# Optimization experiments

Measured on AMD Instinct MI355X. Metric: run time of the kernel, lower is better.

The kernel has to match this reference:

```python
import jax, jax.numpy as jnp
import numpy as np

B, N, K, D = 16, 16384, 16, 256  # batch, num feature tokens, num slots, slot/feature dim
FEAT = 256
LN_EPS = 1e-5


def _ln(x, g, b):
    m = jnp.mean(x, -1, keepdims=True)
    v = jnp.mean((x - m) ** 2, -1, keepdims=True)
    return (x - m) * jax.lax.rsqrt(v + LN_EPS) * g + b


def setup_inputs() -> dict:
    key = jax.random.key(0)
    ks = jax.random.split(key, 18)
    s = 0.02
    return {
        "features": jax.random.normal(ks[0], (B, N, FEAT), jnp.float32),
        "slots_init": jax.random.normal(ks[1], (B, K, D), jnp.float32),
        "g_f": jnp.ones((FEAT,), jnp.float32), "b_f": jnp.zeros((FEAT,), jnp.float32),
        "g_s": jnp.ones((D,), jnp.float32), "b_s": jnp.zeros((D,), jnp.float32),
        "g_m": jnp.ones((D,), jnp.float32), "b_m": jnp.zeros((D,), jnp.float32),
        "Wq": jax.random.normal(ks[2], (D, D), jnp.float32) * s,
        "Wk": jax.random.normal(ks[3], (D, FEAT), jnp.float32) * s,
        "Wv": jax.random.normal(ks[4], (D, FEAT), jnp.float32) * s,
        "w_ih": jax.random.normal(ks[5], (3 * D, D), jnp.float32) * s,
        "w_hh": jax.random.normal(ks[6], (3 * D, D), jnp.float32) * s,
        "b_ih": jnp.zeros((3 * D,), jnp.float32),
        "b_hh": jnp.zeros((3 * D,), jnp.float32),
        "W1": jax.random.normal(ks[7], (4 * D, D), jnp.float32) * s,
        "b1": jnp.zeros((4 * D,), jnp.float32),
        "W2": jax.random.normal(ks[8], (D, 4 * D), jnp.float32) * s,
        "b2": jnp.zeros((D,), jnp.float32),
        "num_src_view": 4,
    }


def reference(features, slots_init, g_f, b_f, g_s, b_s, g_m, b_m, Wq, Wk, Wv,
              w_ih, w_hh, b_ih, b_hh, W1, b1, W2, b2, num_src_view):
    f = _ln(features, g_f, b_f)            # [B,N,FEAT]
    k = f @ Wk.T                            # [B,N,D]
    v = f @ Wv.T                            # [B,N,D]
    scale = float(D) ** -0.5                # num_head = 1, head-mean is identity

    def gru(x, h):  # PyTorch GRUCell math, batched over [B,K]
        gi = x @ w_ih.T + b_ih
        gh = h @ w_hh.T + b_hh
        ir, iz, inn = jnp.split(gi, 3, -1)
        hr, hz, hn = jnp.split(gh, 3, -1)
        r = jax.nn.sigmoid(ir + hr)
        z = jax.nn.sigmoid(iz + hz)
        n = jnp.tanh(inn + r * hn)
        return (1.0 - z) * n + z * h

    def one_iter(slots):
        q = _ln(slots, g_s, b_s) @ Wq.T                         # [B,K,D]
        logits = jnp.einsum('bkd,bnd->bkn', q, k) * scale       # [B,K,N]
        attn = jax.nn.softmax(logits, axis=1)                   # competitive over slots
        attn_wm = attn / (jnp.sum(attn, -1, keepdims=True) + 1.0)  # epsilon = 1.0
        updates = jnp.einsum('bkn,bnd->bkd', attn_wm, v)        # [B,K,D]
        h = gru(updates, slots)
        h = h + (jax.nn.relu(_ln(h, g_m, b_m) @ W1.T + b1) @ W2.T + b2)
        return h, attn

    slots = slots_init
    for _ in range(2):  # num_iter - 1 iterations with straight-through detach trick
        slots, _ = one_iter(slots)
        slots = jax.lax.stop_gradient(slots) + slots_init - jax.lax.stop_gradient(slots_init)
    slots, attn = one_iter(slots)
    return slots, attn
```

## Files before the change

### kernel.cpp

```cpp
#include <hip/hip_runtime.h>
#include <cstdint>
#include <cstddef>

#define BB    16
#define NTOK  16384
#define KS    16
#define DD    256
#define FEATN 256
#define NBLK  32
#define LN_EPS 1e-5f

typedef float        float4v __attribute__((ext_vector_type(4)));
typedef unsigned int uint4v  __attribute__((ext_vector_type(4)));
typedef unsigned int uint2v  __attribute__((ext_vector_type(2)));
typedef __bf16       bf16x8  __attribute__((ext_vector_type(8)));

__device__ __forceinline__ float bflo(unsigned u){ return __builtin_bit_cast(float, u << 16); }
__device__ __forceinline__ float bfhi(unsigned u){ return __builtin_bit_cast(float, u & 0xffff0000u); }
__device__ __forceinline__ unsigned short f2bf(float v){ __bf16 b = (__bf16)v; return __builtin_bit_cast(unsigned short, b); }
__device__ __forceinline__ float sigm(float x){ return 1.f/(1.f + __expf(-x)); }

__global__ void prep_w_kernel(const float* __restrict__ Wv, const float* __restrict__ w_ih,
                              const float* __restrict__ w_hh, const float* __restrict__ W1,
                              const float* __restrict__ W2, const float* __restrict__ Wq,
                              const float* __restrict__ Wk,
                              unsigned short* __restrict__ Wv_t, unsigned short* __restrict__ wih_t,
                              unsigned short* __restrict__ whh_t, unsigned short* __restrict__ W1_t,
                              unsigned short* __restrict__ W2_t, unsigned short* __restrict__ Wq_t,
                              unsigned short* __restrict__ Wk_b)
{
  __shared__ float tile[64][65];
  const int t = blockIdx.x, tid = threadIdx.x;
  const float* src; unsigned short* dst; int R, C, base;
  if      (t < 16)  { src = Wv;   dst = Wv_t;  R = 256;  C = 256;  base = 0;   }
  else if (t < 64)  { src = w_ih; dst = wih_t; R = 768;  C = 256;  base = 16;  }
  else if (t < 112) { src = w_hh; dst = whh_t; R = 768;  C = 256;  base = 64;  }
  else if (t < 176) { src = W1;   dst = W1_t;  R = 1024; C = 256;  base = 112; }
  else if (t < 240) { src = W2;   dst = W2_t;  R = 256;  C = 1024; base = 176; }
  else if (t < 256) { src = Wq;   dst = Wq_t;  R = 256;  C = 256;  base = 240; }
  else {
    const int t2 = t - 256;
    for (int i = tid; i < 4096; i += 256) {
      const int idx = t2*4096 + i;
      Wk_b[idx] = f2bf(Wk[idx]);
    }
    return;
  }
  const int tt = t - base;
  const int tiles_r = R >> 6;
  const int r0 = (tt % tiles_r) * 64, c0 = (tt / tiles_r) * 64;
  const int j = tid & 63, i0 = (tid >> 6) * 16;
  for (int s = 0; s < 16; ++s)
    tile[i0 + s][j] = src[(size_t)(r0 + i0 + s)*C + c0 + j];
  __syncthreads();
  for (int s = 0; s < 16; ++s) {
    const int i = i0 + s;
    dst[(size_t)(c0 + i)*R + r0 + j] = f2bf(tile[j][i]);
  }
}

__device__ __forceinline__ void lnqu_tail_p(
    const float* Vs, float* Ys, float* Qs, float* Pp, float* SUb, float* CBb,
    const float* __restrict__ g_s, const float* __restrict__ b_s,
    const unsigned short* __restrict__ Wq_t, const unsigned short* __restrict__ Wk_b,
    const float* __restrict__ g_f, const float* __restrict__ b_f,
    unsigned short* __restrict__ u_buf, float* __restrict__ su_buf, float* __restrict__ cb_buf,
    int b, int k0, int tid)
{
  const int w = tid >> 6, L = tid & 63;
  {
    const float v0 = Vs[w*256+L], v1 = Vs[w*256+64+L], v2 = Vs[w*256+128+L], v3 = Vs[w*256+192+L];
    float s = v0+v1+v2+v3;
    #pragma unroll
    for (int m = 1; m < 64; m <<= 1) s += __shfl_xor(s, m);
    const float mean = s * (1.f/DD);
    const float d0 = v0-mean, d1 = v1-mean, d2 = v2-mean, d3 = v3-mean;
    float s2 = d0*d0 + d1*d1 + d2*d2 + d3*d3;
    #pragma unroll
    for (int m = 1; m < 64; m <<= 1) s2 += __shfl_xor(s2, m);
    const float rs = rsqrtf(s2 * (1.f/DD) + LN_EPS);
    Ys[L*4+w]       = d0*rs*g_s[L]      + b_s[L];
    Ys[(64+L)*4+w]  = d1*rs*g_s[64+L]   + b_s[64+L];
    Ys[(128+L)*4+w] = d2*rs*g_s[128+L]  + b_s[128+L];
    Ys[(192+L)*4+w] = d3*rs*g_s[192+L]  + b_s[192+L];
  }
  __syncthreads();
  {
    float acc[4][4] = {};
    for (int cc = w*64; cc < w*64+64; ++cc) {
      const float4v xv = *reinterpret_cast<const float4v*>(Ys + cc*4);
      const uint2v wr = *reinterpret_cast<const uint2v*>(Wq_t + (size_t)cc*DD + 4*L);
      const float w0 = bflo(wr[0]), w1 = bfhi(wr[0]), w2 = bflo(wr[1]), w3 = bfhi(wr[1]);
      #pragma unroll
      for (int s = 0; s < 4; ++s) {
        acc[s][0] += xv[s]*w0; acc[s][1] += xv[s]*w1;
        acc[s][2] += xv[s]*w2; acc[s][3] += xv[s]*w3;
      }
    }
    #pragma unroll
    for (int s = 0; s < 4; ++s)
      *reinterpret_cast<float4v*>(Pp + (w*4+s)*256 + 4*L) = *reinterpret_cast<const float4v*>(acc[s]);
  }
  __syncthreads();
  for (int i = tid; i < 4*DD; i += 256) {
    const int kk = i >> 8, d = i & 255;
    Qs[d*4+kk] = Pp[(0*4+kk)*256+d] + Pp[(1*4+kk)*256+d] + Pp[(2*4+kk)*256+d] + Pp[(3*4+kk)*256+d];
  }
  __syncthreads();
  {
    float acc[4][4] = {};
    for (int d = w*64; d < w*64+64; ++d) {
      const float4v xv = *reinterpret_cast<const float4v*>(Qs + d*4);
      const uint2v wr = *reinterpret_cast<const uint2v*>(Wk_b + (size_t)d*DD + 4*L);
      const float w0 = bflo(wr[0]), w1 = bfhi(wr[0]), w2 = bflo(wr[1]), w3 = bfhi(wr[1]);
      #pragma unroll
      for (int s = 0; s < 4; ++s) {
        acc[s][0] += xv[s]*w0; acc[s][1] += xv[s]*w1;
        acc[s][2] += xv[s]*w2; acc[s][3] += xv[s]*w3;
      }
    }
    #pragma unroll
    for (int s = 0; s < 4; ++s)
      *reinterpret_cast<float4v*>(Pp + (w*4+s)*256 + 4*L) = *reinterpret_cast<const float4v*>(acc[s]);
  }
  __syncthreads();
  for (int i = tid; i < 4*DD; i += 256) {
    const int kk = i >> 8, cc = i & 255;
    const float qk = Pp[(0*4+kk)*256+cc] + Pp[(1*4+kk)*256+cc] + Pp[(2*4+kk)*256+cc] + Pp[(3*4+kk)*256+cc];
    const float uv = qk * g_f[cc];
    u_buf[(size_t)(b*KS + k0 + kk)*DD + cc] = f2bf(uv);
    SUb[kk*256+cc] = uv;
    CBb[kk*256+cc] = qk * b_f[cc];
  }
  __syncthreads();
  {
    float s  = SUb[w*256+L] + SUb[w*256+64+L] + SUb[w*256+128+L] + SUb[w*256+192+L];
    float cv = CBb[w*256+L] + CBb[w*256+64+L] + CBb[w*256+128+L] + CBb[w*256+192+L];
    #pragma unroll
    for (int m = 1; m < 64; m <<= 1) { s += __shfl_xor(s, m); cv += __shfl_xor(cv, m); }
    if (L == 0) { su_buf[b*KS + k0 + w] = s; cb_buf[b*KS + k0 + w] = cv; }
  }
}

__global__ void k0_kernel(const float* __restrict__ slots_init,
                          const float* __restrict__ g_s, const float* __restrict__ b_s,
                          const unsigned short* __restrict__ Wq_t, const unsigned short* __restrict__ Wk_b,
                          const float* __restrict__ g_f, const float* __restrict__ b_f,
                          unsigned short* __restrict__ u_buf, float* __restrict__ su_buf,
                          float* __restrict__ cb_buf)
{
  const int b = blockIdx.x >> 2, k0 = (blockIdx.x & 3) * 4;
  const int tid = threadIdx.x;
  __shared__ __align__(16) float Vs[4*DD];
  __shared__ __align__(16) float Ys[DD*4];
  __shared__ __align__(16) float Qs[DD*4];
  __shared__ __align__(16) float Pp[4*4*DD];
  __shared__ __align__(16) float SUb[4*DD];
  __shared__ __align__(16) float CBb[4*DD];
  for (int i = tid; i < 4*DD; i += 256)
    Vs[i] = slots_init[(size_t)(b*KS + k0)*DD + i];
  __syncthreads();
  lnqu_tail_p(Vs, Ys, Qs, Pp, SUb, CBb, g_s, b_s, Wq_t, Wk_b, g_f, b_f,
              u_buf, su_buf, cb_buf, b, k0, tid);
}

template<int MODE, int LAST>
__launch_bounds__(256, 2)
__global__ void phaseA_kernel(const float* __restrict__ feat,
                              unsigned short* __restrict__ xb, float* __restrict__ stats,
                              const unsigned short* __restrict__ u_buf,
                              const float* __restrict__ su_buf,
                              const float* __restrict__ cb_buf,
                              float* __restrict__ P_part,
                              float* __restrict__ S_part,
                              float* __restrict__ R_part,
                              float* __restrict__ attn_out)
{
  __shared__ __align__(16) unsigned int xl[4][128*36];
  __shared__ float ssh[4][16];
  __shared__ float rsh[4][16];

  const int b   = blockIdx.x / NBLK;
  const int blk = blockIdx.x - b*NBLK;
  const int tid = threadIdx.x;
  const int w = tid >> 6;
  const int l = tid & 63;
  const int c = l & 15;
  const int g = l >> 4;

  bf16x8 ufrag[8];
  {
    const bf16x8* up = reinterpret_cast<const bf16x8*>(u_buf + (size_t)(b*KS + c)*DD);
    #pragma unroll
    for (int kk = 0; kk < 8; ++kk) ufrag[kk] = up[4*kk + g];
  }
  const float su_c = su_buf[b*KS + c];
  const float cb_c = cb_buf[b*KS + c];

  float4v Pacc[16];
  #pragma unroll
  for (int t = 0; t < 16; ++t) Pacc[t] = (float4v){0.f,0.f,0.f,0.f};
  float S_acc = 0.f, R_acc = 0.f;

  unsigned int* myxl = xl[w];
  const int rbase = 8*(c>>2) + (c&3);

  for (int pass = 0; pass < 4; ++pass) {
    const int n0 = blk*(NTOK/NBLK) + pass*128 + w*32;
    float4v Ct[2];
    float m_t[2], rs_t[2];

    if constexpr (MODE == 1) {
      bf16x8 xr0[8], xr1[8];
      float2 st0, st1;
      {
        const size_t row0 = (size_t)b*NTOK + (size_t)(n0 + rbase);
        const size_t row1 = row0 + 4;
        const bf16x8* p0v = reinterpret_cast<const bf16x8*>(xb + row0*FEATN);
        const bf16x8* p1v = reinterpret_cast<const bf16x8*>(xb + row1*FEATN);
        #pragma unroll
        for (int kk = 0; kk < 8; ++kk) { xr0[kk] = p0v[4*kk + g]; xr1[kk] = p1v[4*kk + g]; }
        st0 = *reinterpret_cast<const float2*>(stats + row0*2);
        st1 = *reinterpret_cast<const float2*>(stats + row1*2);
      }
      #pragma unroll
      for (int tp = 0; tp < 2; ++tp) {
        const int nloc = rbase + 4*tp;
        float4v Cacc = (float4v){0.f,0.f,0.f,0.f};
        #pragma unroll
        for (int kk = 0; kk < 8; ++kk) {
          const bf16x8 af = tp ? xr1[kk] : xr0[kk];
          const uint4v ad = __builtin_bit_cast(uint4v, af);
          const int pb = (16*kk + 4*g)*36 + nloc;
          myxl[pb      ] = ad[0];
          myxl[pb + 36 ] = ad[1];
          myxl[pb + 72 ] = ad[2];
          myxl[pb + 108] = ad[3];
          Cacc = __builtin_amdgcn_mfma_f32_16x16x32_bf16(af, ufrag[kk], Cacc, 0, 0, 0);
        }
        m_t[tp]  = tp ? st1.x : st0.x;
        rs_t[tp] = tp ? st1.y : st0.y;
        Ct[tp]   = Cacc;
      }
    } else {
      #pragma unroll
      for (int tp = 0; tp < 2; ++tp) {
        const int nloc = rbase + 4*tp;
        const size_t row = (size_t)b*NTOK + (size_t)(n0 + nloc);
        const float* fr = feat + row*FEATN;
        float4v xf[16];
        #pragma unroll
        for (int kk = 0; kk < 8; ++kk) {
          xf[2*kk]   = *reinterpret_cast<const float4v*>(fr + 32*kk + 8*g);
          xf[2*kk+1] = *reinterpret_cast<const float4v*>(fr + 32*kk + 8*g + 4);
        }
        unsigned short* xw = xb + row*FEATN;
        float sum = 0.f, sq = 0.f;
        float4v Cacc = (float4v){0.f,0.f,0.f,0.f};
        #pragma unroll
        for (int kk = 0; kk < 8; ++kk) {
          const float4v x0 = xf[2*kk], x1 = xf[2*kk+1];
          sum += x0[0]+x0[1]+x0[2]+x0[3] + x1[0]+x1[1]+x1[2]+x1[3];
          sq  += x0[0]*x0[0]+x0[1]*x0[1]+x0[2]*x0[2]+x0[3]*x0[3]
               + x1[0]*x1[0]+x1[1]*x1[1]+x1[2]*x1[2]+x1[3]*x1[3];
          bf16x8 af;
          af[0]=(__bf16)x0[0]; af[1]=(__bf16)x0[1]; af[2]=(__bf16)x0[2]; af[3]=(__bf16)x0[3];
          af[4]=(__bf16)x1[0]; af[5]=(__bf16)x1[1]; af[6]=(__bf16)x1[2]; af[7]=(__bf16)x1[3];
          *reinterpret_cast<bf16x8*>(xw + 32*kk + 8*g) = af;
          const uint4v ad = __builtin_bit_cast(uint4v, af);
          const int pb = (16*kk + 4*g)*36 + nloc;
          myxl[pb      ] = ad[0];
          myxl[pb + 36 ] = ad[1];
          myxl[pb + 72 ] = ad[2];
          myxl[pb + 108] = ad[3];
          Cacc = __builtin_amdgcn_mfma_f32_16x16x32_bf16(af, ufrag[kk], Cacc, 0, 0, 0);
        }
        sum += __shfl_xor(sum,16); sum += __shfl_xor(sum,32);
        sq  += __shfl_xor(sq ,16); sq  += __shfl_xor(sq ,32);
        const float mean = sum * (1.f/FEATN);
        const float var  = sq  * (1.f/FEATN) - mean*mean;
        m_t[tp]  = mean;
        rs_t[tp] = rsqrtf(var + LN_EPS);
        float2 st; st.x = m_t[tp]; st.y = rs_t[tp];
        *reinterpret_cast<float2*>(stats + row*2) = st;
        Ct[tp] = Cacc;
      }
    }

    float arr[8];
    #pragma unroll
    for (int tp = 0; tp < 2; ++tp) {
      float lv[4], rsr[4], mr[4];
      #pragma unroll
      for (int r = 0; r < 4; ++r) {
        const int src = 4*g + r;
        rsr[r] = __shfl(rs_t[tp], src);
        mr[r]  = __shfl(m_t[tp],  src);
        lv[r]  = 0.0625f * (rsr[r]*(Ct[tp][r] - mr[r]*su_c) + cb_c);
      }
      float a_[4];
      #pragma unroll
      for (int r = 0; r < 4; ++r) {
        float v = lv[r];
        v = fmaxf(v, __shfl_xor(v,1));
        v = fmaxf(v, __shfl_xor(v,2));
        v = fmaxf(v, __shfl_xor(v,4));
        v = fmaxf(v, __shfl_xor(v,8));
        const float e = __expf(lv[r] - v);
        float s = e;
        s += __shfl_xor(s,1);
        s += __shfl_xor(s,2);
        s += __shfl_xor(s,4);
        s += __shfl_xor(s,8);
        const float a = e / s;
        a_[r] = a;
        S_acc += a;
        R_acc += a * rsr[r] * mr[r];
        arr[4*tp + r] = a * rsr[r];
      }
      if (LAST) {
        float4v av = {a_[0], a_[1], a_[2], a_[3]};
        *reinterpret_cast<float4v*>(attn_out + (size_t)(b*KS + c)*NTOK + (size_t)(n0 + 8*g + 4*tp)) = av;
      }
    }
    bf16x8 afrag;
    #pragma unroll
    for (int j = 0; j < 8; ++j) afrag[j] = (__bf16)arr[j];

    #pragma unroll
    for (int t = 0; t < 16; ++t) {
      const unsigned int* rp = &myxl[(t*8 + (c>>1))*36 + 8*g];
      const uint4v q0 = *reinterpret_cast<const uint4v*>(rp);
      const uint4v q1 = *reinterpret_cast<const uint4v*>(rp + 4);
      const unsigned int sel = (c & 1) ? 0x07060302u : 0x05040100u;
      uint4v bd;
      bd[0] = __builtin_amdgcn_perm(q0[1], q0[0], sel);
      bd[1] = __builtin_amdgcn_perm(q0[3], q0[2], sel);
      bd[2] = __builtin_amdgcn_perm(q1[1], q1[0], sel);
      bd[3] = __builtin_amdgcn_perm(q1[3], q1[2], sel);
      const bf16x8 bfrag = __builtin_bit_cast(bf16x8, bd);
      Pacc[t] = __builtin_amdgcn_mfma_f32_16x16x32_bf16(afrag, bfrag, Pacc[t], 0, 0, 0);
    }
  }

  S_acc += __shfl_xor(S_acc,16); S_acc += __shfl_xor(S_acc,32);
  R_acc += __shfl_xor(R_acc,16); R_acc += __shfl_xor(R_acc,32);
  if (g == 0) { ssh[w][c] = S_acc; rsh[w][c] = R_acc; }

  float* pf = reinterpret_cast<float*>(myxl);
  #pragma unroll
  for (int t = 0; t < 16; ++t) {
    #pragma unroll
    for (int r = 0; r < 4; ++r) pf[(4*g + r)*256 + t*16 + c] = Pacc[t][r];
  }
  __syncthreads();
  {
    float* outp = P_part + (size_t)blockIdx.x * (KS*DD);
    const float* p0 = reinterpret_cast<const float*>(&xl[0][0]);
    const float* p1 = p0 + 4608;
    const float* p2 = p0 + 9216;
    const float* p3 = p0 + 13824;
    for (int i = tid; i < KS*DD; i += 256) outp[i] = p0[i]+p1[i]+p2[i]+p3[i];
    if (tid < KS) {
      S_part[blockIdx.x*KS + tid] = ssh[0][tid]+ssh[1][tid]+ssh[2][tid]+ssh[3][tid];
      R_part[blockIdx.x*KS + tid] = rsh[0][tid]+rsh[1][tid]+rsh[2][tid]+rsh[3][tid];
    }
  }
}

template<int LAST, int NEXT>
__global__ void fusedB_kernel(const float* __restrict__ P_part, const float* __restrict__ S_part,
                              const float* __restrict__ R_part, const float* __restrict__ slots_in,
                              const float* __restrict__ g_f, const float* __restrict__ b_f,
                              const unsigned short* __restrict__ Wv_t,
                              const unsigned short* __restrict__ wih_t,
                              const unsigned short* __restrict__ whh_t,
                              const float* __restrict__ b_ih, const float* __restrict__ b_hh,
                              const float* __restrict__ g_m, const float* __restrict__ b_m,
                              const unsigned short* __restrict__ W1_t, const float* __restrict__ b1,
                              const unsigned short* __restrict__ W2_t, const float* __restrict__ b2v,
                              const float* __restrict__ g_s, const float* __restrict__ b_s,
                              const unsigned short* __restrict__ Wq_t,
                              const unsigned short* __restrict__ Wk_b,
                              float* __restrict__ slots_next, float* __restrict__ out_slots,
                              unsigned short* __restrict__ u_buf, float* __restrict__ su_buf,
                              float* __restrict__ cb_buf)
{
  const int b = blockIdx.x >> 4, k = blockIdx.x & 15;
  const int tid = threadIdx.x;
  const int w = tid >> 6, L = tid & 63;

  __shared__ __align__(16) float arena[9984];
  __shared__ float SRsh[2];
  __shared__ float redsh[8];

  float* Pp    = arena;
  float* Hsh   = arena + 6144;
  float* Tsh   = arena + 6400;
  float* Ush   = arena + 6656;
  float* Gish  = arena + 6912;
  float* Ghsh  = arena + 7680;
  float* Hpsh  = arena + 8448;
  float* Ysh   = arena + 8704;
  float* Hidsh = arena + 8960;

  Hsh[tid] = slots_in[(size_t)(b*KS + k)*DD + tid];
  if (tid < 64) {
    const int p = tid & 31;
    const float* sp = (tid < 32) ? S_part : R_part;
    float v = sp[(b*NBLK + p)*KS + k];
    v += __shfl_xor(v, 1); v += __shfl_xor(v, 2); v += __shfl_xor(v, 4);
    v += __shfl_xor(v, 8); v += __shfl_xor(v, 16);
    if (p == 0) SRsh[tid >> 5] = v;
  }
  __syncthreads();

  {
    const float S = SRsh[0], R = SRsh[1];
    const float inv = 1.f / (S + 1.f);
    const float* pb = P_part + (size_t)(b*NBLK)*KS*DD + (size_t)k*DD + tid;
    float p0 = 0.f, p1 = 0.f, p2 = 0.f, p3 = 0.f;
    #pragma unroll
    for (int p = 0; p < NBLK; p += 4) {
      p0 += pb[(size_t)(p+0)*KS*DD];
      p1 += pb[(size_t)(p+1)*KS*DD];
      p2 += pb[(size_t)(p+2)*KS*DD];
      p3 += pb[(size_t)(p+3)*KS*DD];
    }
    const float P = (p0 + p1) + (p2 + p3);
    Tsh[tid] = (g_f[tid]*(P - R) + S*b_f[tid]) * inv;
  }
  __syncthreads();

  {
    const int c0 = 4*L;
    float a0 = 0.f, a1 = 0.f, a2 = 0.f, a3 = 0.f;
    for (int cc = w*64; cc < w*64+64; ++cc) {
      const float x = Tsh[cc];
      const uint2v wr = *reinterpret_cast<const uint2v*>(Wv_t + (size_t)cc*DD + c0);
      a0 += x*bflo(wr[0]); a1 += x*bfhi(wr[0]);
      a2 += x*bflo(wr[1]); a3 += x*bfhi(wr[1]);
    }
    float4v av = {a0, a1, a2, a3};
    *reinterpret_cast<float4v*>(Pp + w*256 + c0) = av;
  }
  __syncthreads();
  Ush[tid] = Pp[tid] + Pp[256+tid] + Pp[512+tid] + Pp[768+tid];
  __syncthreads();

  {
    const int c0 = 4*L;
    float ai[3][4] = {}, ah[3][4] = {};
    for (int cc = w*64; cc < w*64+64; ++cc) {
      const float xi = Ush[cc], xh = Hsh[cc];
      #pragma unroll
      for (int c = 0; c < 3; ++c) {
        const uint2v wi = *reinterpret_cast<const uint2v*>(wih_t + (size_t)cc*768 + c0 + 256*c);
        const uint2v wh = *reinterpret_cast<const uint2v*>(whh_t + (size_t)cc*768 + c0 + 256*c);
        ai[c][0] += xi*bflo(wi[0]); ai[c][1] += xi*bfhi(wi[0]);
        ai[c][2] += xi*bflo(wi[1]); ai[c][3] += xi*bfhi(wi[1]);
        ah[c][0] += xh*bflo(wh[0]); ah[c][1] += xh*bfhi(wh[0]);
        ah[c][2] += xh*bflo(wh[1]); ah[c][3] += xh*bfhi(wh[1]);
      }
    }
    #pragma unroll
    for (int c = 0; c < 3; ++c) {
      *reinterpret_cast<float4v*>(Pp + w*768 + 256*c + c0)        = *reinterpret_cast<const float4v*>(ai[c]);
      *reinterpret_cast<float4v*>(Pp + 3072 + w*768 + 256*c + c0) = *reinterpret_cast<const float4v*>(ah[c]);
    }
  }
  __syncthreads();
  for (int j = tid; j < 768; j += 256) {
    Gish[j] = b_ih[j] + Pp[j] + Pp[768+j] + Pp[1536+j] + Pp[2304+j];
    Ghsh[j] = b_hh[j] + Pp[3072+j] + Pp[3840+j] + Pp[4608+j] + Pp[5376+j];
  }
  __syncthreads();

  {
    const int d = tid;
    const float r = sigm(Gish[d] + Ghsh[d]);
    const float z = sigm(Gish[256+d] + Ghsh[256+d]);
    const float n = tanhf(Gish[512+d] + r*Ghsh[512+d]);
    const float hp = (1.f - z)*n + z*Hsh[d];
    Hpsh[d] = hp;
    float s = hp;
    #pragma unroll
    for (int m = 1; m < 64; m <<= 1) s += __shfl_xor(s, m);
    if (L == 0) redsh[w] = s;
    __syncthreads();
    const float mean = (redsh[0]+redsh[1]+redsh[2]+redsh[3]) * (1.f/DD);
    const float dv = hp - mean;
    float s2 = dv*dv;
    #pragma unroll
    for (int m = 1; m < 64; m <<= 1) s2 += __shfl_xor(s2, m);
    if (L == 0) redsh[4+w] = s2;
    __syncthreads();
    const float var = (redsh[4]+redsh[5]+redsh[6]+redsh[7]) * (1.f/DD);
    Ysh[d] = dv * rsqrtf(var + LN_EPS) * g_m[d] + b_m[d];
  }
  __syncthreads();

  {
    const int c0 = 4*L;
    float a[4][4] = {};
    for (int cc = w*64; cc < w*64+64; ++cc) {
      const float x = Ysh[cc];
      #pragma unroll
      for (int c = 0; c < 4; ++c) {
        const uint2v wr = *reinterpret_cast<const uint2v*>(W1_t + (size_t)cc*1024 + c0 + 256*c);
        a[c][0] += x*bflo(wr[0]); a[c][1] += x*bfhi(wr[0]);
        a[c][2] += x*bflo(wr[1]); a[c][3] += x*bfhi(wr[1]);
      }
    }
    #pragma unroll
    for (int c = 0; c < 4; ++c)
      *reinterpret_cast<float4v*>(Pp + w*1024 + 256*c + c0) = *reinterpret_cast<const float4v*>(a[c]);
  }
  __syncthreads();
  for (int j = tid; j < 1024; j += 256)
    Hidsh[j] = fmaxf(b1[j] + Pp[j] + Pp[1024+j] + Pp[2048+j] + Pp[3072+j], 0.f);
  __syncthreads();

  {
    const int c0 = 4*L;
    float a0 = 0.f, a1 = 0.f, a2 = 0.f, a3 = 0.f;
    for (int cc = w*256; cc < w*256+256; ++cc) {
      const float x = Hidsh[cc];
      const uint2v wr = *reinterpret_cast<const uint2v*>(W2_t + (size_t)cc*DD + c0);
      a0 += x*bflo(wr[0]); a1 += x*bfhi(wr[0]);
      a2 += x*bflo(wr[1]); a3 += x*bfhi(wr[1]);
    }
    float4v av = {a0, a1, a2, a3};
    *reinterpret_cast<float4v*>(Pp + w*256 + c0) = av;
  }
  __syncthreads();
  {
    const int d = tid;
    const float v = b2v[d] + Pp[d] + Pp[256+d] + Pp[512+d] + Pp[768+d] + Hpsh[d];
    Tsh[d] = v;
    slots_next[(size_t)(b*KS + k)*DD + d] = v;
    if (LAST) out_slots[(size_t)(b*KS + k)*DD + d] = v;
  }

  if constexpr (NEXT) {
    __syncthreads();
    {
      const float v = Tsh[tid];
      float s = v;
      #pragma unroll
      for (int m = 1; m < 64; m <<= 1) s += __shfl_xor(s, m);
      if (L == 0) redsh[w] = s;
      __syncthreads();
      const float mean = (redsh[0]+redsh[1]+redsh[2]+redsh[3]) * (1.f/DD);
      const float dv = v - mean;
      float s2 = dv*dv;
      #pragma unroll
      for (int m = 1; m < 64; m <<= 1) s2 += __shfl_xor(s2, m);
      if (L == 0) redsh[4+w] = s2;
      __syncthreads();
      const float var = (redsh[4]+redsh[5]+redsh[6]+redsh[7]) * (1.f/DD);
      Ush[tid] = dv * rsqrtf(var + LN_EPS) * g_s[tid] + b_s[tid];
    }
    __syncthreads();
    {
      const int c0 = 4*L;
      float a0 = 0.f, a1 = 0.f, a2 = 0.f, a3 = 0.f;
      for (int cc = w*64; cc < w*64+64; ++cc) {
        const float x = Ush[cc];
        const uint2v wr = *reinterpret_cast<const uint2v*>(Wq_t + (size_t)cc*DD + c0);
        a0 += x*bflo(wr[0]); a1 += x*bfhi(wr[0]);
        a2 += x*bflo(wr[1]); a3 += x*bfhi(wr[1]);
      }
      float4v av = {a0, a1, a2, a3};
      *reinterpret_cast<float4v*>(Pp + w*256 + c0) = av;
    }
    __syncthreads();
    Hsh[tid] = Pp[tid] + Pp[256+tid] + Pp[512+tid] + Pp[768+tid];
    __syncthreads();
    {
      const int c0 = 4*L;
      float a0 = 0.f, a1 = 0.f, a2 = 0.f, a3 = 0.f;
      for (int dd = w*64; dd < w*64+64; ++dd) {
        const float x = Hsh[dd];
        const uint2v wr = *reinterpret_cast<const uint2v*>(Wk_b + (size_t)dd*DD + c0);
        a0 += x*bflo(wr[0]); a1 += x*bfhi(wr[0]);
        a2 += x*bflo(wr[1]); a3 += x*bfhi(wr[1]);
      }
      float4v av = {a0, a1, a2, a3};
      *reinterpret_cast<float4v*>(Pp + w*256 + c0) = av;
    }
    __syncthreads();
    {
      const int cidx = tid;
      const float qk = Pp[cidx] + Pp[256+cidx] + Pp[512+cidx] + Pp[768+cidx];
      const float uv = qk * g_f[cidx];
      u_buf[(size_t)(b*KS + k)*DD + cidx] = f2bf(uv);
      float s  = uv;
      float cv = qk * b_f[cidx];
      #pragma unroll
      for (int m = 1; m < 64; m <<= 1) { s += __shfl_xor(s, m); cv += __shfl_xor(cv, m); }
      if (L == 0) { redsh[w] = s; redsh[4+w] = cv; }
      __syncthreads();
      if (tid == 0) {
        su_buf[b*KS + k] = redsh[0]+redsh[1]+redsh[2]+redsh[3];
        cb_buf[b*KS + k] = redsh[4]+redsh[5]+redsh[6]+redsh[7];
      }
    }
  }
}

extern "C" void kernel_launch(void* const* d_in, const int* in_sizes, int n_in,
                              void* d_out, int out_size, void* d_ws, size_t ws_size,
                              hipStream_t stream)
{
  const float* features   = (const float*)d_in[0];
  const float* slots_init = (const float*)d_in[1];
  const float* g_f = (const float*)d_in[2];
  const float* b_f = (const float*)d_in[3];
  const float* g_s = (const float*)d_in[4];
  const float* b_s = (const float*)d_in[5];
  const float* g_m = (const float*)d_in[6];
  const float* b_m = (const float*)d_in[7];
  const float* Wq  = (const float*)d_in[8];
  const float* Wk  = (const float*)d_in[9];
  const float* Wv  = (const float*)d_in[10];
  const float* w_ih = (const float*)d_in[11];
  const float* w_hh = (const float*)d_in[12];
  const float* b_ih = (const float*)d_in[13];
  const float* b_hh = (const float*)d_in[14];
  const float* W1  = (const float*)d_in[15];
  const float* b1  = (const float*)d_in[16];
  const float* W2  = (const float*)d_in[17];
  const float* b2  = (const float*)d_in[18];

  float* out_slots = (float*)d_out;
  float* out_attn  = out_slots + (size_t)BB*KS*DD;

  char* ws = (char*)d_ws;
  size_t off = 0;
  auto alloc = [&](size_t bytes) -> void* {
    void* p = ws + off;
    off += (bytes + 255) & ~(size_t)255;
    return p;
  };
  unsigned short* u_buf  = (unsigned short*)alloc((size_t)BB*KS*DD*2);
  float*          su_buf = (float*)alloc((size_t)BB*KS*4);
  float*          cb_buf = (float*)alloc((size_t)BB*KS*4);
  float*          P_part = (float*)alloc((size_t)BB*NBLK*KS*DD*4);
  float*          S_part = (float*)alloc((size_t)BB*NBLK*KS*4);
  float*          R_part = (float*)alloc((size_t)BB*NBLK*KS*4);
  float*          slots_ws = (float*)alloc((size_t)BB*KS*DD*4);
  unsigned short* Wv_t  = (unsigned short*)alloc((size_t)256*256*2);
  unsigned short* wih_t = (unsigned short*)alloc((size_t)256*768*2);
  unsigned short* whh_t = (unsigned short*)alloc((size_t)256*768*2);
  unsigned short* W1_t  = (unsigned short*)alloc((size_t)256*1024*2);
  unsigned short* W2_t  = (unsigned short*)alloc((size_t)1024*256*2);
  unsigned short* Wq_t  = (unsigned short*)alloc((size_t)256*256*2);
  unsigned short* Wk_b  = (unsigned short*)alloc((size_t)256*256*2);
  float*          stats = (float*)alloc((size_t)BB*NTOK*2*4);
  unsigned short* xb    = (unsigned short*)alloc((size_t)BB*NTOK*FEATN*2);
  (void)in_sizes; (void)n_in; (void)out_size; (void)ws_size;

  prep_w_kernel<<<272, 256, 0, stream>>>(Wv, w_ih, w_hh, W1, W2, Wq, Wk,
                                         Wv_t, wih_t, whh_t, W1_t, W2_t, Wq_t, Wk_b);
  k0_kernel<<<BB*4, 256, 0, stream>>>(slots_init, g_s, b_s, Wq_t, Wk_b, g_f, b_f,
                                      u_buf, su_buf, cb_buf);

  phaseA_kernel<0,0><<<BB*NBLK, 256, 0, stream>>>(features, xb, stats, u_buf, su_buf, cb_buf,
                                                  P_part, S_part, R_part, out_attn);
  fusedB_kernel<0,1><<<BB*KS, 256, 0, stream>>>(P_part, S_part, R_part, slots_init, g_f, b_f,
                                                Wv_t, wih_t, whh_t, b_ih, b_hh, g_m, b_m,
                                                W1_t, b1, W2_t, b2, g_s, b_s, Wq_t, Wk_b,
                                                slots_ws, out_slots, u_buf, su_buf, cb_buf);
  phaseA_kernel<1,0><<<BB*NBLK, 256, 0, stream>>>(features, xb, stats, u_buf, su_buf, cb_buf,
                                                  P_part, S_part, R_part, out_attn);
  fusedB_kernel<0,1><<<BB*KS, 256, 0, stream>>>(P_part, S_part, R_part, slots_ws, g_f, b_f,
                                                Wv_t, wih_t, whh_t, b_ih, b_hh, g_m, b_m,
                                                W1_t, b1, W2_t, b2, g_s, b_s, Wq_t, Wk_b,
                                                slots_ws, out_slots, u_buf, su_buf, cb_buf);
  phaseA_kernel<1,1><<<BB*NBLK, 256, 0, stream>>>(features, xb, stats, u_buf, su_buf, cb_buf,
                                                  P_part, S_part, R_part, out_attn);
  fusedB_kernel<1,0><<<BB*KS, 256, 0, stream>>>(P_part, S_part, R_part, slots_ws, g_f, b_f,
                                                Wv_t, wih_t, whh_t, b_ih, b_hh, g_m, b_m,
                                                W1_t, b1, W2_t, b2, g_s, b_s, Wq_t, Wk_b,
                                                slots_ws, out_slots, u_buf, su_buf, cb_buf);
}
```

Before: 390.0 us.

## Halve phaseA per-wave token tile, double block count, raise occupancy

Each wave in phaseA now handles 16 tokens per pass instead of 32. The grid doubles to 64 blocks per batch, the LDS staging buffer is halved, and the launch bound for MODE 1 is raised to 3 blocks per CU. The attention-times-X accumulation switches to the 16x16x16 bf16 MFMA where that builtin exists, and the P partial reduction is done in two halves to fit the smaller LDS. The goal is more parallelism and occupancy in the memory-bound token pass, at the cost of twice as many partial sums for fusedB to reduce and more MFMA instructions per token.

```diff
diff --git a/kernel.cpp b/kernel.cpp
--- a/kernel.cpp
+++ b/kernel.cpp
@@ -7,13 +7,14 @@
 #define KS    16
 #define DD    256
 #define FEATN 256
-#define NBLK  32
+#define NBLK  64
 #define LN_EPS 1e-5f
 
 typedef float        float4v __attribute__((ext_vector_type(4)));
 typedef unsigned int uint4v  __attribute__((ext_vector_type(4)));
 typedef unsigned int uint2v  __attribute__((ext_vector_type(2)));
 typedef __bf16       bf16x8  __attribute__((ext_vector_type(8)));
+typedef short        short4v __attribute__((ext_vector_type(4)));
 
 __device__ __forceinline__ float bflo(unsigned u){ return __builtin_bit_cast(float, u << 16); }
 __device__ __forceinline__ float bfhi(unsigned u){ return __builtin_bit_cast(float, u & 0xffff0000u); }
@@ -165,7 +166,7 @@
 }
 
 template<int MODE, int LAST>
-__launch_bounds__(256, 2)
+__launch_bounds__(256, (MODE==0) ? 2 : 3)
 __global__ void phaseA_kernel(const float* __restrict__ feat,
                               unsigned short* __restrict__ xb, float* __restrict__ stats,
                               const unsigned short* __restrict__ u_buf,
@@ -176,7 +177,7 @@
                               float* __restrict__ R_part,
                               float* __restrict__ attn_out)
 {
-  __shared__ __align__(16) unsigned int xl[4][128*36];
+  __shared__ __align__(16) unsigned int xl[4][128*18];
   __shared__ float ssh[4][16];
   __shared__ float rsh[4][16];
 
@@ -201,170 +202,176 @@
   #pragma unroll
   for (int t = 0; t < 16; ++t) Pacc[t] = (float4v){0.f,0.f,0.f,0.f};
   float S_acc = 0.f, R_acc = 0.f;
-
   unsigned int* myxl = xl[w];
-  const int rbase = 8*(c>>2) + (c&3);
 
   for (int pass = 0; pass < 4; ++pass) {
-    const int n0 = blk*(NTOK/NBLK) + pass*128 + w*32;
-    float4v Ct[2];
-    float m_t[2], rs_t[2];
-
-    if constexpr (MODE == 1) {
-      bf16x8 xr0[8], xr1[8];
-      float2 st0, st1;
+    const int n0 = blk*(NTOK/NBLK) + pass*64 + w*16;
+    const size_t row = (size_t)b*NTOK + (size_t)(n0 + c);
+    float4v Cacc = (float4v){0.f,0.f,0.f,0.f};
+    float m_c, rs_c;
+
+    if constexpr (MODE == 0) {
+      const float* fr = feat + row*FEATN;
+      unsigned short* xw = xb + row*FEATN;
+      float4v xf[16];
+      #pragma unroll
+      for (int kk = 0; kk < 8; ++kk) {
+        xf[2*kk]   = *reinterpret_cast<const float4v*>(fr + 32*kk + 8*g);
+        xf[2*kk+1] = *reinterpret_cast<const float4v*>(fr + 32*kk + 8*g + 4);
+      }
+      float sum = 0.f, sq = 0.f;
+      #pragma unroll
+      for (int kk = 0; kk < 8; ++kk) {
+        const float4v x0 = xf[2*kk], x1 = xf[2*kk+1];
+        sum += x0[0]+x0[1]+x0[2]+x0[3] + x1[0]+x1[1]+x1[2]+x1[3];
+        sq  += x0[0]*x0[0]+x0[1]*x0[1]+x0[2]*x0[2]+x0[3]*x0[3]
+             + x1[0]*x1[0]+x1[1]*x1[1]+x1[2]*x1[2]+x1[3]*x1[3];
+        bf16x8 af;
+        af[0]=(__bf16)x0[0]; af[1]=(__bf16)x0[1]; af[2]=(__bf16)x0[2]; af[3]=(__bf16)x0[3];
+        af[4]=(__bf16)x1[0]; af[5]=(__bf16)x1[1]; af[6]=(__bf16)x1[2]; af[7]=(__bf16)x1[3];
+        *reinterpret_cast<bf16x8*>(xw + 32*kk + 8*g) = af;
+        const uint4v ad = __builtin_bit_cast(uint4v, af);
+        const int pb = (16*kk + 4*g)*18 + c;
+        myxl[pb     ] = ad[0];
+        myxl[pb + 18] = ad[1];
+        myxl[pb + 36] = ad[2];
+        myxl[pb + 54] = ad[3];
+        Cacc = __builtin_amdgcn_mfma_f32_16x16x32_bf16(af, ufrag[kk], Cacc, 0, 0, 0);
+      }
+      sum += __shfl_xor(sum,16); sum += __shfl_xor(sum,32);
+      sq  += __shfl_xor(sq ,16); sq  += __shfl_xor(sq ,32);
+      m_c = sum * (1.f/FEATN);
+      const float var = sq * (1.f/FEATN) - m_c*m_c;
+      rs_c = rsqrtf(var + LN_EPS);
+      if (g == 0) {
+        float2 st; st.x = m_c; st.y = rs_c;
+        *reinterpret_cast<float2*>(stats + row*2) = st;
+      }
+    } else {
+      const unsigned short* xr0p = xb + row*FEATN;
+      bf16x8 xr[8];
       {
-        const size_t row0 = (size_t)b*NTOK + (size_t)(n0 + rbase);
-        const size_t row1 = row0 + 4;
-        const bf16x8* p0v = reinterpret_cast<const bf16x8*>(xb + row0*FEATN);
-        const bf16x8* p1v = reinterpret_cast<const bf16x8*>(xb + row1*FEATN);
+        const bf16x8* pv = reinterpret_cast<const bf16x8*>(xr0p);
         #pragma unroll
-        for (int kk = 0; kk < 8; ++kk) { xr0[kk] = p0v[4*kk + g]; xr1[kk] = p1v[4*kk + g]; }
-        st0 = *reinterpret_cast<const float2*>(stats + row0*2);
-        st1 = *reinterpret_cast<const float2*>(stats + row1*2);
-      }
-      #pragma unroll
-      for (int tp = 0; tp < 2; ++tp) {
-        const int nloc = rbase + 4*tp;
-        float4v Cacc = (float4v){0.f,0.f,0.f,0.f};
-        #pragma unroll
-        for (int kk = 0; kk < 8; ++kk) {
-          const bf16x8 af = tp ? xr1[kk] : xr0[kk];
-          const uint4v ad = __builtin_bit_cast(uint4v, af);
-          const int pb = (16*kk + 4*g)*36 + nloc;
-          myxl[pb      ] = ad[0];
-          myxl[pb + 36 ] = ad[1];
-          myxl[pb + 72 ] = ad[2];
-          myxl[pb + 108] = ad[3];
-          Cacc = __builtin_amdgcn_mfma_f32_16x16x32_bf16(af, ufrag[kk], Cacc, 0, 0, 0);
-        }
-        m_t[tp]  = tp ? st1.x : st0.x;
-        rs_t[tp] = tp ? st1.y : st0.y;
-        Ct[tp]   = Cacc;
-      }
-    } else {
-      #pragma unroll
-      for (int tp = 0; tp < 2; ++tp) {
-        const int nloc = rbase + 4*tp;
-        const size_t row = (size_t)b*NTOK + (size_t)(n0 + nloc);
-        const float* fr = feat + row*FEATN;
-        float4v xf[16];
-        #pragma unroll
-        for (int kk = 0; kk < 8; ++kk) {
-          xf[2*kk]   = *reinterpret_cast<const float4v*>(fr + 32*kk + 8*g);
-          xf[2*kk+1] = *reinterpret_cast<const float4v*>(fr + 32*kk + 8*g + 4);
-        }
-        unsigned short* xw = xb + row*FEATN;
-        float sum = 0.f, sq = 0.f;
-        float4v Cacc = (float4v){0.f,0.f,0.f,0.f};
-        #pragma unroll
-        for (int kk = 0; kk < 8; ++kk) {
-          const float4v x0 = xf[2*kk], x1 = xf[2*kk+1];
-          sum += x0[0]+x0[1]+x0[2]+x0[3] + x1[0]+x1[1]+x1[2]+x1[3];
-          sq  += x0[0]*x0[0]+x0[1]*x0[1]+x0[2]*x0[2]+x0[3]*x0[3]
-               + x1[0]*x1[0]+x1[1]*x1[1]+x1[2]*x1[2]+x1[3]*x1[3];
-          bf16x8 af;
-          af[0]=(__bf16)x0[0]; af[1]=(__bf16)x0[1]; af[2]=(__bf16)x0[2]; af[3]=(__bf16)x0[3];
-          af[4]=(__bf16)x1[0]; af[5]=(__bf16)x1[1]; af[6]=(__bf16)x1[2]; af[7]=(__bf16)x1[3];
-          *reinterpret_cast<bf16x8*>(xw + 32*kk + 8*g) = af;
-          const uint4v ad = __builtin_bit_cast(uint4v, af);
-          const int pb = (16*kk + 4*g)*36 + nloc;
-          myxl[pb      ] = ad[0];
-          myxl[pb + 36 ] = ad[1];
-          myxl[pb + 72 ] = ad[2];
-          myxl[pb + 108] = ad[3];
-          Cacc = __builtin_amdgcn_mfma_f32_16x16x32_bf16(af, ufrag[kk], Cacc, 0, 0, 0);
-        }
-        sum += __shfl_xor(sum,16); sum += __shfl_xor(sum,32);
-        sq  += __shfl_xor(sq ,16); sq  += __shfl_xor(sq ,32);
-        const float mean = sum * (1.f/FEATN);
-        const float var  = sq  * (1.f/FEATN) - mean*mean;
-        m_t[tp]  = mean;
-        rs_t[tp] = rsqrtf(var + LN_EPS);
-        float2 st; st.x = m_t[tp]; st.y = rs_t[tp];
-        *reinterpret_cast<float2*>(stats + row*2) = st;
-        Ct[tp] = Cacc;
-      }
-    }
-
-    float arr[8];
-    #pragma unroll
-    for (int tp = 0; tp < 2; ++tp) {
-      float lv[4], rsr[4], mr[4];
-      #pragma unroll
-      for (int r = 0; r < 4; ++r) {
-        const int src = 4*g + r;
-        rsr[r] = __shfl(rs_t[tp], src);
-        mr[r]  = __shfl(m_t[tp],  src);
-        lv[r]  = 0.0625f * (rsr[r]*(Ct[tp][r] - mr[r]*su_c) + cb_c);
-      }
-      float a_[4];
-      #pragma unroll
-      for (int r = 0; r < 4; ++r) {
-        float v = lv[r];
-        v = fmaxf(v, __shfl_xor(v,1));
-        v = fmaxf(v, __shfl_xor(v,2));
-        v = fmaxf(v, __shfl_xor(v,4));
-        v = fmaxf(v, __shfl_xor(v,8));
-        const float e = __expf(lv[r] - v);
-        float s = e;
-        s += __shfl_xor(s,1);
-        s += __shfl_xor(s,2);
-        s += __shfl_xor(s,4);
-        s += __shfl_xor(s,8);
-        const float a = e / s;
-        a_[r] = a;
-        S_acc += a;
-        R_acc += a * rsr[r] * mr[r];
-        arr[4*tp + r] = a * rsr[r];
-      }
-      if (LAST) {
-        float4v av = {a_[0], a_[1], a_[2], a_[3]};
-        *reinterpret_cast<float4v*>(attn_out + (size_t)(b*KS + c)*NTOK + (size_t)(n0 + 8*g + 4*tp)) = av;
-      }
-    }
-    bf16x8 afrag;
-    #pragma unroll
-    for (int j = 0; j < 8; ++j) afrag[j] = (__bf16)arr[j];
-
+        for (int kk = 0; kk < 8; ++kk) xr[kk] = pv[4*kk + g];
+      }
+      const float2 st = *reinterpret_cast<const float2*>(stats + row*2);
+      m_c = st.x; rs_c = st.y;
+      #pragma unroll
+      for (int kk = 0; kk < 8; ++kk) {
+        const bf16x8 af = xr[kk];
+        const uint4v ad = __builtin_bit_cast(uint4v, af);
+        const int pb = (16*kk + 4*g)*18 + c;
+        myxl[pb     ] = ad[0];
+        myxl[pb + 18] = ad[1];
+        myxl[pb + 36] = ad[2];
+        myxl[pb + 54] = ad[3];
+        Cacc = __builtin_amdgcn_mfma_f32_16x16x32_bf16(af, ufrag[kk], Cacc, 0, 0, 0);
+      }
+    }
+
+    float arr[4], a_[4];
+    #pragma unroll
+    for (int r = 0; r < 4; ++r) {
+      const int src = 4*g + r;
+      const float rsr = __shfl(rs_c, src);
+      const float mrr = __shfl(m_c,  src);
+      const float lv = 0.0625f * (rsr*(Cacc[r] - mrr*su_c) + cb_c);
+      float v = lv;
+      v = fmaxf(v, __shfl_xor(v,1));
+      v = fmaxf(v, __shfl_xor(v,2));
+      v = fmaxf(v, __shfl_xor(v,4));
+      v = fmaxf(v, __shfl_xor(v,8));
+      const float e = __expf(lv - v);
+      float s = e;
+      s += __shfl_xor(s,1);
+      s += __shfl_xor(s,2);
+      s += __shfl_xor(s,4);
+      s += __shfl_xor(s,8);
+      const float a = e / s;
+      a_[r] = a;
+      S_acc += a;
+      R_acc += a * rsr * mrr;
+      arr[r] = a * rsr;
+    }
+    if (LAST) {
+      float4v av = {a_[0], a_[1], a_[2], a_[3]};
+      *reinterpret_cast<float4v*>(attn_out + (size_t)(b*KS + c)*NTOK + (size_t)(n0 + 4*g)) = av;
+    }
+
+#if __has_builtin(__builtin_amdgcn_mfma_f32_16x16x16bf16_1k)
+    short4v afrag;
+    afrag[0] = (short)f2bf(arr[0]); afrag[1] = (short)f2bf(arr[1]);
+    afrag[2] = (short)f2bf(arr[2]); afrag[3] = (short)f2bf(arr[3]);
+    const unsigned int sel = (c & 1) ? 0x07060302u : 0x05040100u;
     #pragma unroll
     for (int t = 0; t < 16; ++t) {
-      const unsigned int* rp = &myxl[(t*8 + (c>>1))*36 + 8*g];
-      const uint4v q0 = *reinterpret_cast<const uint4v*>(rp);
-      const uint4v q1 = *reinterpret_cast<const uint4v*>(rp + 4);
-      const unsigned int sel = (c & 1) ? 0x07060302u : 0x05040100u;
-      uint4v bd;
-      bd[0] = __builtin_amdgcn_perm(q0[1], q0[0], sel);
-      bd[1] = __builtin_amdgcn_perm(q0[3], q0[2], sel);
-      bd[2] = __builtin_amdgcn_perm(q1[1], q1[0], sel);
-      bd[3] = __builtin_amdgcn_perm(q1[3], q1[2], sel);
+      const unsigned int* rp = &myxl[(t*8 + (c>>1))*18 + 4*g];
+      const uint2v d0 = *reinterpret_cast<const uint2v*>(rp);
+      const uint2v d1 = *reinterpret_cast<const uint2v*>(rp + 2);
+      uint2v bd;
+      bd[0] = __builtin_amdgcn_perm(d0[1], d0[0], sel);
+      bd[1] = __builtin_amdgcn_perm(d1[1], d1[0], sel);
+      const short4v bfrag = __builtin_bit_cast(short4v, bd);
+      Pacc[t] = __builtin_amdgcn_mfma_f32_16x16x16bf16_1k(afrag, bfrag, Pacc[t], 0, 0, 0);
+    }
+#else
+    bf16x8 afrag8;
+    #pragma unroll
+    for (int j = 0; j < 8; ++j) {
+      const int srcl = c + 16*(2*g + (j>>2));
+      const float v = __shfl(arr[j & 3], srcl);
+      afrag8[j] = (g < 2) ? (__bf16)v : (__bf16)0.f;
+    }
+    const unsigned int sel = (c & 1) ? 0x07060302u : 0x05040100u;
+    #pragma unroll
+    for (int t = 0; t < 16; ++t) {
+      uint4v bd = (uint4v){0u,0u,0u,0u};
+      if (g < 2) {
+        const unsigned int* rp = &myxl[(t*8 + (c>>1))*18 + 8*g];
+        const uint2v d0 = *reinterpret_cast<const uint2v*>(rp);
+        const uint2v d1 = *reinterpret_cast<const uint2v*>(rp + 2);
+        const uint2v d2 = *reinterpret_cast<const uint2v*>(rp + 4);
+        const uint2v d3 = *reinterpret_cast<const uint2v*>(rp + 6);
+        bd[0] = __builtin_amdgcn_perm(d0[1], d0[0], sel);
+        bd[1] = __builtin_amdgcn_perm(d1[1], d1[0], sel);
+        bd[2] = __builtin_amdgcn_perm(d2[1], d2[0], sel);
+        bd[3] = __builtin_amdgcn_perm(d3[1], d3[0], sel);
+      }
       const bf16x8 bfrag = __builtin_bit_cast(bf16x8, bd);
-      Pacc[t] = __builtin_amdgcn_mfma_f32_16x16x32_bf16(afrag, bfrag, Pacc[t], 0, 0, 0);
-    }
+      Pacc[t] = __builtin_amdgcn_mfma_f32_16x16x32_bf16(afrag8, bfrag, Pacc[t], 0, 0, 0);
+    }
+#endif
   }
 
   S_acc += __shfl_xor(S_acc,16); S_acc += __shfl_xor(S_acc,32);
   R_acc += __shfl_xor(R_acc,16); R_acc += __shfl_xor(R_acc,32);
   if (g == 0) { ssh[w][c] = S_acc; rsh[w][c] = R_acc; }
 
-  float* pf = reinterpret_cast<float*>(myxl);
+  float* pf = reinterpret_cast<float*>(&xl[w][0]);
   #pragma unroll
-  for (int t = 0; t < 16; ++t) {
-    #pragma unroll
-    for (int r = 0; r < 4; ++r) pf[(4*g + r)*256 + t*16 + c] = Pacc[t][r];
-  }
-  __syncthreads();
-  {
-    float* outp = P_part + (size_t)blockIdx.x * (KS*DD);
+  for (int half = 0; half < 2; ++half) {
+    __syncthreads();
+    #pragma unroll
+    for (int t = 0; t < 8; ++t) {
+      #pragma unroll
+      for (int r = 0; r < 4; ++r)
+        pf[(4*g + r)*128 + t*16 + c] = Pacc[half*8 + t][r];
+    }
+    __syncthreads();
+    float* outp = P_part + (size_t)blockIdx.x * (KS*DD) + half*128;
     const float* p0 = reinterpret_cast<const float*>(&xl[0][0]);
-    const float* p1 = p0 + 4608;
-    const float* p2 = p0 + 9216;
-    const float* p3 = p0 + 13824;
-    for (int i = tid; i < KS*DD; i += 256) outp[i] = p0[i]+p1[i]+p2[i]+p3[i];
-    if (tid < KS) {
-      S_part[blockIdx.x*KS + tid] = ssh[0][tid]+ssh[1][tid]+ssh[2][tid]+ssh[3][tid];
-      R_part[blockIdx.x*KS + tid] = rsh[0][tid]+rsh[1][tid]+rsh[2][tid]+rsh[3][tid];
-    }
+    const float* p1 = p0 + 2304;
+    const float* p2 = p0 + 4608;
+    const float* p3 = p0 + 6912;
+    for (int i = tid; i < 2048; i += 256) {
+      const int rowk = i >> 7, rem = i & 127;
+      outp[rowk*256 + rem] = p0[i] + p1[i] + p2[i] + p3[i];
+    }
+  }
+  if (tid < KS) {
+    S_part[blockIdx.x*KS + tid] = ssh[0][tid]+ssh[1][tid]+ssh[2][tid]+ssh[3][tid];
+    R_part[blockIdx.x*KS + tid] = rsh[0][tid]+rsh[1][tid]+rsh[2][tid]+rsh[3][tid];
   }
 }
 
@@ -405,13 +412,14 @@
   float* Hidsh = arena + 8960;
 
   Hsh[tid] = slots_in[(size_t)(b*KS + k)*DD + tid];
-  if (tid < 64) {
-    const int p = tid & 31;
-    const float* sp = (tid < 32) ? S_part : R_part;
+  if (tid < 128) {
+    const int which = tid >> 6;
+    const int p = tid & 63;
+    const float* sp = which ? R_part : S_part;
     float v = sp[(b*NBLK + p)*KS + k];
-    v += __shfl_xor(v, 1); v += __shfl_xor(v, 2); v += __shfl_xor(v, 4);
-    v += __shfl_xor(v, 8); v += __shfl_xor(v, 16);
-    if (p == 0) SRsh[tid >> 5] = v;
+    #pragma unroll
+    for (int m = 1; m < 64; m <<= 1) v += __shfl_xor(v, m);
+    if (p == 0) SRsh[which] = v;
   }
   __syncthreads();
 
@@ -420,7 +428,7 @@
     const float inv = 1.f / (S + 1.f);
     const float* pb = P_part + (size_t)(b*NBLK)*KS*DD + (size_t)k*DD + tid;
     float p0 = 0.f, p1 = 0.f, p2 = 0.f, p3 = 0.f;
-    #pragma unroll
+    #pragma unroll 4
     for (int p = 0; p < NBLK; p += 4) {
       p0 += pb[(size_t)(p+0)*KS*DD];
       p1 += pb[(size_t)(p+1)*KS*DD];
```

Result: slower. 414.9 us (+6.4%).

## Double-buffer bf16 feature loads across passes and split MFMA accumulator chains

Applied to the files above, without the earlier changes.

In the MODE 1 path, the four-pass loop is software-pipelined. The next pass's bf16 feature rows and stats are loaded into alternate register buffers while the current pass computes, which hides global load latency. Both paths split the logits MFMA accumulation into two independent chains to shorten the dependency chain. The P_part reduction loop's unroll factor is also reduced to 2. The double buffering raises register pressure and may lower occupancy.

```diff
diff --git a/kernel.cpp b/kernel.cpp
--- a/kernel.cpp
+++ b/kernel.cpp
@@ -205,88 +205,7 @@
   unsigned int* myxl = xl[w];
   const int rbase = 8*(c>>2) + (c&3);
 
-  for (int pass = 0; pass < 4; ++pass) {
-    const int n0 = blk*(NTOK/NBLK) + pass*128 + w*32;
-    float4v Ct[2];
-    float m_t[2], rs_t[2];
-
-    if constexpr (MODE == 1) {
-      bf16x8 xr0[8], xr1[8];
-      float2 st0, st1;
-      {
-        const size_t row0 = (size_t)b*NTOK + (size_t)(n0 + rbase);
-        const size_t row1 = row0 + 4;
-        const bf16x8* p0v = reinterpret_cast<const bf16x8*>(xb + row0*FEATN);
-        const bf16x8* p1v = reinterpret_cast<const bf16x8*>(xb + row1*FEATN);
-        #pragma unroll
-        for (int kk = 0; kk < 8; ++kk) { xr0[kk] = p0v[4*kk + g]; xr1[kk] = p1v[4*kk + g]; }
-        st0 = *reinterpret_cast<const float2*>(stats + row0*2);
-        st1 = *reinterpret_cast<const float2*>(stats + row1*2);
-      }
-      #pragma unroll
-      for (int tp = 0; tp < 2; ++tp) {
-        const int nloc = rbase + 4*tp;
-        float4v Cacc = (float4v){0.f,0.f,0.f,0.f};
-        #pragma unroll
-        for (int kk = 0; kk < 8; ++kk) {
-          const bf16x8 af = tp ? xr1[kk] : xr0[kk];
-          const uint4v ad = __builtin_bit_cast(uint4v, af);
-          const int pb = (16*kk + 4*g)*36 + nloc;
-          myxl[pb      ] = ad[0];
-          myxl[pb + 36 ] = ad[1];
-          myxl[pb + 72 ] = ad[2];
-          myxl[pb + 108] = ad[3];
-          Cacc = __builtin_amdgcn_mfma_f32_16x16x32_bf16(af, ufrag[kk], Cacc, 0, 0, 0);
-        }
-        m_t[tp]  = tp ? st1.x : st0.x;
-        rs_t[tp] = tp ? st1.y : st0.y;
-        Ct[tp]   = Cacc;
-      }
-    } else {
-      #pragma unroll
-      for (int tp = 0; tp < 2; ++tp) {
-        const int nloc = rbase + 4*tp;
-        const size_t row = (size_t)b*NTOK + (size_t)(n0 + nloc);
-        const float* fr = feat + row*FEATN;
-        float4v xf[16];
-        #pragma unroll
-        for (int kk = 0; kk < 8; ++kk) {
-          xf[2*kk]   = *reinterpret_cast<const float4v*>(fr + 32*kk + 8*g);
-          xf[2*kk+1] = *reinterpret_cast<const float4v*>(fr + 32*kk + 8*g + 4);
-        }
-        unsigned short* xw = xb + row*FEATN;
-        float sum = 0.f, sq = 0.f;
-        float4v Cacc = (float4v){0.f,0.f,0.f,0.f};
-        #pragma unroll
-        for (int kk = 0; kk < 8; ++kk) {
-          const float4v x0 = xf[2*kk], x1 = xf[2*kk+1];
-          sum += x0[0]+x0[1]+x0[2]+x0[3] + x1[0]+x1[1]+x1[2]+x1[3];
-          sq  += x0[0]*x0[0]+x0[1]*x0[1]+x0[2]*x0[2]+x0[3]*x0[3]
-               + x1[0]*x1[0]+x1[1]*x1[1]+x1[2]*x1[2]+x1[3]*x1[3];
-          bf16x8 af;
-          af[0]=(__bf16)x0[0]; af[1]=(__bf16)x0[1]; af[2]=(__bf16)x0[2]; af[3]=(__bf16)x0[3];
-          af[4]=(__bf16)x1[0]; af[5]=(__bf16)x1[1]; af[6]=(__bf16)x1[2]; af[7]=(__bf16)x1[3];
-          *reinterpret_cast<bf16x8*>(xw + 32*kk + 8*g) = af;
-          const uint4v ad = __builtin_bit_cast(uint4v, af);
-          const int pb = (16*kk + 4*g)*36 + nloc;
-          myxl[pb      ] = ad[0];
-          myxl[pb + 36 ] = ad[1];
-          myxl[pb + 72 ] = ad[2];
-          myxl[pb + 108] = ad[3];
-          Cacc = __builtin_amdgcn_mfma_f32_16x16x32_bf16(af, ufrag[kk], Cacc, 0, 0, 0);
-        }
-        sum += __shfl_xor(sum,16); sum += __shfl_xor(sum,32);
-        sq  += __shfl_xor(sq ,16); sq  += __shfl_xor(sq ,32);
-        const float mean = sum * (1.f/FEATN);
-        const float var  = sq  * (1.f/FEATN) - mean*mean;
-        m_t[tp]  = mean;
-        rs_t[tp] = rsqrtf(var + LN_EPS);
-        float2 st; st.x = m_t[tp]; st.y = rs_t[tp];
-        *reinterpret_cast<float2*>(stats + row*2) = st;
-        Ct[tp] = Cacc;
-      }
-    }
-
+  auto tailpass = [&](int n0, const float4v* Ct, const float* m_t, const float* rs_t) {
     float arr[8];
     #pragma unroll
     for (int tp = 0; tp < 2; ++tp) {
@@ -340,6 +259,105 @@
       bd[3] = __builtin_amdgcn_perm(q1[3], q1[2], sel);
       const bf16x8 bfrag = __builtin_bit_cast(bf16x8, bd);
       Pacc[t] = __builtin_amdgcn_mfma_f32_16x16x32_bf16(afrag, bfrag, Pacc[t], 0, 0, 0);
+    }
+  };
+
+  if constexpr (MODE == 1) {
+    auto ldp = [&](int pass, bf16x8* r0, bf16x8* r1, float2& s0, float2& s1) {
+      const int n0 = blk*(NTOK/NBLK) + pass*128 + w*32;
+      const size_t row0 = (size_t)b*NTOK + (size_t)(n0 + rbase);
+      const bf16x8* p0v = reinterpret_cast<const bf16x8*>(xb + row0*FEATN);
+      const bf16x8* p1v = reinterpret_cast<const bf16x8*>(xb + (row0 + 4)*FEATN);
+      #pragma unroll
+      for (int kk = 0; kk < 8; ++kk) { r0[kk] = p0v[4*kk + g]; r1[kk] = p1v[4*kk + g]; }
+      s0 = *reinterpret_cast<const float2*>(stats + row0*2);
+      s1 = *reinterpret_cast<const float2*>(stats + (row0 + 4)*2);
+    };
+    auto dop = [&](int pass, const bf16x8* xr0, const bf16x8* xr1, float2 st0, float2 st1) {
+      const int n0 = blk*(NTOK/NBLK) + pass*128 + w*32;
+      float4v Ct[2]; float m_t[2], rs_t[2];
+      #pragma unroll
+      for (int tp = 0; tp < 2; ++tp) {
+        const int nloc = rbase + 4*tp;
+        float4v Ca = (float4v){0.f,0.f,0.f,0.f}, Cb = Ca;
+        #pragma unroll
+        for (int kk = 0; kk < 8; ++kk) {
+          const bf16x8 af = tp ? xr1[kk] : xr0[kk];
+          const uint4v ad = __builtin_bit_cast(uint4v, af);
+          const int pb = (16*kk + 4*g)*36 + nloc;
+          myxl[pb      ] = ad[0];
+          myxl[pb + 36 ] = ad[1];
+          myxl[pb + 72 ] = ad[2];
+          myxl[pb + 108] = ad[3];
+          if (kk & 1) Cb = __builtin_amdgcn_mfma_f32_16x16x32_bf16(af, ufrag[kk], Cb, 0, 0, 0);
+          else        Ca = __builtin_amdgcn_mfma_f32_16x16x32_bf16(af, ufrag[kk], Ca, 0, 0, 0);
+        }
+        Ct[tp] = Ca + Cb;
+        m_t[tp]  = tp ? st1.x : st0.x;
+        rs_t[tp] = tp ? st1.y : st0.y;
+      }
+      tailpass(n0, Ct, m_t, rs_t);
+    };
+
+    bf16x8 A0[8], A1[8], B0[8], B1[8];
+    float2 sa0, sa1, sb0, sb1;
+    ldp(0, A0, A1, sa0, sa1);
+    ldp(1, B0, B1, sb0, sb1);
+    dop(0, A0, A1, sa0, sa1);
+    ldp(2, A0, A1, sa0, sa1);
+    dop(1, B0, B1, sb0, sb1);
+    ldp(3, B0, B1, sb0, sb1);
+    dop(2, A0, A1, sa0, sa1);
+    dop(3, B0, B1, sb0, sb1);
+  } else {
+    for (int pass = 0; pass < 4; ++pass) {
+      const int n0 = blk*(NTOK/NBLK) + pass*128 + w*32;
+      float4v Ct[2];
+      float m_t[2], rs_t[2];
+      #pragma unroll
+      for (int tp = 0; tp < 2; ++tp) {
+        const int nloc = rbase + 4*tp;
+        const size_t row = (size_t)b*NTOK + (size_t)(n0 + nloc);
+        const float* fr = feat + row*FEATN;
+        float4v xf[16];
+        #pragma unroll
+        for (int kk = 0; kk < 8; ++kk) {
+          xf[2*kk]   = *reinterpret_cast<const float4v*>(fr + 32*kk + 8*g);
+          xf[2*kk+1] = *reinterpret_cast<const float4v*>(fr + 32*kk + 8*g + 4);
+        }
+        unsigned short* xw = xb + row*FEATN;
+        float sum = 0.f, sq = 0.f;
+        float4v Ca = (float4v){0.f,0.f,0.f,0.f}, Cb = Ca;
+        #pragma unroll
+        for (int kk = 0; kk < 8; ++kk) {
+          const float4v x0 = xf[2*kk], x1 = xf[2*kk+1];
+          sum += x0[0]+x0[1]+x0[2]+x0[3] + x1[0]+x1[1]+x1[2]+x1[3];
+          sq  += x0[0]*x0[0]+x0[1]*x0[1]+x0[2]*x0[2]+x0[3]*x0[3]
+               + x1[0]*x1[0]+x1[1]*x1[1]+x1[2]*x1[2]+x1[3]*x1[3];
+          bf16x8 af;
+          af[0]=(__bf16)x0[0]; af[1]=(__bf16)x0[1]; af[2]=(__bf16)x0[2]; af[3]=(__bf16)x0[3];
+          af[4]=(__bf16)x1[0]; af[5]=(__bf16)x1[1]; af[6]=(__bf16)x1[2]; af[7]=(__bf16)x1[3];
+          *reinterpret_cast<bf16x8*>(xw + 32*kk + 8*g) = af;
+          const uint4v ad = __builtin_bit_cast(uint4v, af);
+          const int pb = (16*kk + 4*g)*36 + nloc;
+          myxl[pb      ] = ad[0];
+          myxl[pb + 36 ] = ad[1];
+          myxl[pb + 72 ] = ad[2];
+          myxl[pb + 108] = ad[3];
+          if (kk & 1) Cb = __builtin_amdgcn_mfma_f32_16x16x32_bf16(af, ufrag[kk], Cb, 0, 0, 0);
+          else        Ca = __builtin_amdgcn_mfma_f32_16x16x32_bf16(af, ufrag[kk], Ca, 0, 0, 0);
+        }
+        sum += __shfl_xor(sum,16); sum += __shfl_xor(sum,32);
+        sq  += __shfl_xor(sq ,16); sq  += __shfl_xor(sq ,32);
+        const float mean = sum * (1.f/FEATN);
+        const float var  = sq  * (1.f/FEATN) - mean*mean;
+        m_t[tp]  = mean;
+        rs_t[tp] = rsqrtf(var + LN_EPS);
+        float2 st; st.x = m_t[tp]; st.y = rs_t[tp];
+        *reinterpret_cast<float2*>(stats + row*2) = st;
+        Ct[tp] = Ca + Cb;
+      }
+      tailpass(n0, Ct, m_t, rs_t);
     }
   }
 
@@ -420,7 +438,7 @@
     const float inv = 1.f / (S + 1.f);
     const float* pb = P_part + (size_t)(b*NBLK)*KS*DD + (size_t)k*DD + tid;
     float p0 = 0.f, p1 = 0.f, p2 = 0.f, p3 = 0.f;
-    #pragma unroll
+    #pragma unroll 2
     for (int p = 0; p < NBLK; p += 4) {
       p0 += pb[(size_t)(p+0)*KS*DD];
       p1 += pb[(size_t)(p+1)*KS*DD];
```

New measurement: 394.9 us. No clear change (+1.2%).
